# Performance work log

Measured on AMD Instinct MI355X. Metric: run time of the kernel, lower is better.

## Reference

```python
import jax, jax.numpy as jnp
import numpy as np

N = 10000      # nodes
E = 320000     # edges (before self loops)
IN = 256
HID = 64
H = 8
OUT = 64
NEG_SLOPE = 0.2


def setup_inputs() -> dict:
    key = jax.random.key(0)
    ks = jax.random.split(key, 12)
    def glorot(k, shape):
        fan = sum(shape) if len(shape) == 2 else int(np.prod(shape))
        return jax.random.normal(k, shape, jnp.float32) * np.sqrt(2.0 / fan)
    x = jax.random.normal(ks[0], (N, IN), jnp.float32)
    edge_index = jax.random.randint(ks[1], (2, E), 0, N, jnp.int32)
    # positive weights so log2 is finite
    edge_weight = jax.random.uniform(ks[2], (E,), jnp.float32, 0.1, 1.0)
    return {
        'x': x, 'edge_index': edge_index, 'edge_weight': edge_weight,
        'W1': glorot(ks[3], (IN, H * HID)),
        'as1': glorot(ks[4], (H, HID)), 'ad1': glorot(ks[5], (H, HID)),
        'b1': jnp.zeros((H * HID,), jnp.float32),
        'W2': glorot(ks[6], (H * HID, H * OUT)),
        'as2': glorot(ks[7], (H, OUT)), 'ad2': glorot(ks[8], (H, OUT)),
        'b2': jnp.zeros((H * OUT,), jnp.float32),
    }


def _gat_conv(x, src, dst, log2_ew, W, att_src, att_dst, bias, heads, ch):
    n = x.shape[0]
    h = (x @ W).reshape(n, heads, ch)                      # [N,H,C]
    al_src = jnp.einsum('nhc,hc->nh', h, att_src)          # [N,H]
    al_dst = jnp.einsum('nhc,hc->nh', h, att_dst)
    alpha = al_src[src] + al_dst[dst]                      # [E,H]
    alpha = jax.nn.leaky_relu(alpha, NEG_SLOPE)
    alpha = alpha + log2_ew[:, None]
    # segment softmax over destination nodes (self loops ensure nonempty segments)
    amax = jax.ops.segment_max(alpha, dst, num_segments=n)
    ex = jnp.exp(alpha - amax[dst])
    denom = jax.ops.segment_sum(ex, dst, num_segments=n)
    alpha = ex / denom[dst]                                # [E,H]
    msg = h[src] * alpha[:, :, None]                       # [E,H,C]
    out = jax.ops.segment_sum(msg, dst, num_segments=n)    # [N,H,C]
    return out.reshape(n, heads * ch) + bias


def reference(x, edge_index, edge_weight, W1, as1, ad1, b1, W2, as2, ad2, b2):
    n = x.shape[0]
    # add self loops with fill_value = 1.0 (log2(1) = 0)
    loops = jnp.arange(n, dtype=edge_index.dtype)
    src = jnp.concatenate([edge_index[0], loops])
    dst = jnp.concatenate([edge_index[1], loops])
    ew = jnp.concatenate([edge_weight, jnp.ones((n,), edge_weight.dtype)])
    log2_ew = jnp.log2(ew)
    h = _gat_conv(x, src, dst, log2_ew, W1, as1, ad1, b1, H, HID)
    h = jax.nn.relu(h)  # dropout skipped (eval mode)
    out = _gat_conv(h, src, dst, log2_ew, W2, as2, ad2, b2, H, OUT)
    return out
```

## Files before the change

### kernel.cpp

```cpp
#include <hip/hip_runtime.h>
#include <hip/hip_bf16.h>

#define NN 10000
#define EE 320000
#define ETOT (EE + NN)
#define CIN 256
#define HC 512
#define NHEAD 8
#define NEG 0.2f

#define SX (NN * CIN)
#define SW1 (CIN * HC)
#define SW2 (HC * HC)
#define SATT (6 * 512)

using bf16x8 = __attribute__((ext_vector_type(8))) short;
using f32x4 = __attribute__((ext_vector_type(4))) float;
typedef unsigned short u16;
typedef unsigned int u32;

__device__ __forceinline__ u16 f2bf(float f) {
  __hip_bfloat16 b = __float2bfloat16(f);
  return *(u16*)&b;
}
__device__ __forceinline__ float bflo(u32 p) { return __uint_as_float(p << 16); }
__device__ __forceinline__ float bfhi(u32 p) { return __uint_as_float(p & 0xFFFF0000u); }

__global__ void zdetect_k(const u16* __restrict__ x, int* __restrict__ flag,
                          int* __restrict__ counts) {
  int i = blockIdx.x * blockDim.x + threadIdx.x;
  if (i < NN) counts[i] = 0;
  if (blockIdx.x == 0 && threadIdx.x < 64) {
    int bad = 0;
    for (int j = threadIdx.x; j < 512; j += 64) {
      unsigned e = (x[j] >> 7) & 0xFFu;
      if (e >= 0xC8u) bad = 1;
    }
    unsigned long long b = __ballot(bad);
    if (threadIdx.x == 0) *flag = (b == 0ull) ? 1 : 0;
  }
}

__global__ void cvt_count_k(const void* __restrict__ x,
                            const void* a0, const void* a1, const void* a2,
                            const void* a3, const void* a4, const void* a5,
                            const int* __restrict__ ei,
                            u16* __restrict__ xb, float* __restrict__ attf,
                            int* __restrict__ counts, const int* __restrict__ flag) {
  int i = blockIdx.x * blockDim.x + threadIdx.x;
  const bool bf = (*flag != 0);
  if (i < SX) {
    xb[i] = bf ? ((const u16*)x)[i] : f2bf(((const float*)x)[i]);
  } else if (i < SX + SATT) {
    int j = i - SX;
    const void* ps[6] = {a0, a1, a2, a3, a4, a5};
    const void* p = ps[j >> 9];
    int k = j & 511;
    attf[j] = bf ? __bfloat162float(((const __hip_bfloat16*)p)[k])
                 : ((const float*)p)[k];
  }
  if (i < ETOT) {
    int d = (i < EE) ? ei[EE + i] : (i - EE);
    atomicAdd(&counts[d], 1);
  }
}

__global__ __launch_bounds__(256) void wtrans_k(const void* __restrict__ w1,
                                                const void* __restrict__ w2,
                                                u16* __restrict__ w1t,
                                                u16* __restrict__ w2t,
                                                const int* __restrict__ flag) {
  __shared__ u16 tile[64][72];
  int b = blockIdx.x;
  const void* src;
  u16* dst;
  int K, tk, tn;
  if (b < 32) { src = w1; dst = w1t; K = CIN; tk = (b >> 3) * 64; tn = (b & 7) * 64; }
  else { b -= 32; src = w2; dst = w2t; K = HC; tk = (b >> 3) * 64; tn = (b & 7) * 64; }
  const bool bf = (*flag != 0);
  const int t = threadIdx.x;
  const int r = t >> 2, cb = (t & 3) * 16;
  if (bf) {
    const u16* s = (const u16*)src + (size_t)(tk + r) * HC + tn + cb;
    *(int4*)&tile[r][cb] = ((const int4*)s)[0];
    *(int4*)&tile[r][cb + 8] = ((const int4*)s)[1];
  } else {
    const float* s = (const float*)src + (size_t)(tk + r) * HC + tn + cb;
#pragma unroll
    for (int j = 0; j < 16; j++) tile[r][cb + j] = f2bf(s[j]);
  }
  __syncthreads();
  union { u16 o[16]; int4 v[2]; } u;
#pragma unroll
  for (int j = 0; j < 16; j++) u.o[j] = tile[cb + j][r];
  int4* dp = (int4*)(dst + (size_t)(tn + r) * K + tk + cb);
  dp[0] = u.v[0];
  dp[1] = u.v[1];
}

__global__ __launch_bounds__(1024) void scan_k(const int* __restrict__ counts,
                                               int* __restrict__ rowptr,
                                               int* __restrict__ wcur) {
  __shared__ int buf[1024];
  const int t = threadIdx.x;
  int loc[10];
  int s = 0;
#pragma unroll
  for (int j = 0; j < 10; j++) {
    int i = t * 10 + j;
    s += (i < NN) ? counts[i] : 0;
    loc[j] = s;
  }
  buf[t] = s;
  __syncthreads();
  for (int off = 1; off < 1024; off <<= 1) {
    int v = (t >= off) ? buf[t - off] : 0;
    __syncthreads();
    buf[t] += v;
    __syncthreads();
  }
  int base = (t > 0) ? buf[t - 1] : 0;
  int prev = 0;
#pragma unroll
  for (int j = 0; j < 10; j++) {
    int i = t * 10 + j;
    if (i < NN) {
      rowptr[i + 1] = base + loc[j];
      wcur[i] = base + prev;
    }
    prev = loc[j];
  }
  if (t == 0) rowptr[0] = 0;
}

__global__ void fill_k(const int* __restrict__ ei, const void* __restrict__ ew,
                       const int* __restrict__ flag, int* __restrict__ wcur,
                       int* __restrict__ esrc, float* __restrict__ elw) {
  int e = blockIdx.x * blockDim.x + threadIdx.x;
  if (e >= ETOT) return;
  int s, d;
  float lw;
  if (e < EE) {
    s = ei[e];
    d = ei[EE + e];
    float w = (*flag) ? __bfloat162float(((const __hip_bfloat16*)ew)[e])
                      : ((const float*)ew)[e];
    lw = log2f(w);
  } else {
    s = d = e - EE;
    lw = 0.f;
  }
  int pos = atomicAdd(&wcur[d], 1);
  esrc[pos] = s;
  elw[pos] = lw;
}

#define BM 128
#define BN 64
#define BK 32
#define APAD 40
#define BPAD 40

__global__ __launch_bounds__(256) void gemm_mfma(const u16* __restrict__ A,
                                                 const u16* __restrict__ Wt,
                                                 const float* __restrict__ as_w,
                                                 const float* __restrict__ ad_w,
                                                 u16* __restrict__ hb,
                                                 float* __restrict__ alsrc,
                                                 float* __restrict__ aldst,
                                                 int M, int K) {
  __shared__ u16 As[BM * APAD];
  __shared__ u16 Bs[BN * BPAD];
  const int head = blockIdx.x;
  const int bm = blockIdx.y * BM, bn = head * BN;
  const int t = threadIdx.x;
  const int wave = t >> 6, lane = t & 63;
  const int l15 = lane & 15, quad = lane >> 4;
  f32x4 acc[2][4] = {};
  for (int k0 = 0; k0 < K; k0 += BK) {
    {
      int row = t >> 1, half = t & 1;
      int gr = bm + row;
      int4 v0 = make_int4(0, 0, 0, 0), v1 = v0;
      if (gr < M) {
        const int4* gp = (const int4*)(A + (size_t)gr * K + k0 + half * 16);
        v0 = gp[0];
        v1 = gp[1];
      }
      int4* lp = (int4*)(As + row * APAD + half * 16);
      lp[0] = v0;
      lp[1] = v1;
    }
    {
      int row = t >> 2, kq = (t & 3) * 8;
      *(int4*)(Bs + row * BPAD + kq) =
          *(const int4*)(Wt + (size_t)(bn + row) * K + k0 + kq);
    }
    __syncthreads();
    bf16x8 af[2], bfr[4];
#pragma unroll
    for (int rt = 0; rt < 2; rt++)
      af[rt] = *(const bf16x8*)(As + (wave * 32 + rt * 16 + l15) * APAD + quad * 8);
#pragma unroll
    for (int ct = 0; ct < 4; ct++)
      bfr[ct] = *(const bf16x8*)(Bs + (ct * 16 + l15) * BPAD + quad * 8);
#pragma unroll
    for (int rt = 0; rt < 2; rt++)
#pragma unroll
      for (int ct = 0; ct < 4; ct++)
        acc[rt][ct] = __builtin_amdgcn_mfma_f32_16x16x32_bf16(af[rt], bfr[ct],
                                                              acc[rt][ct], 0, 0, 0);
    __syncthreads();
  }
  float asw[4], adw[4];
#pragma unroll
  for (int ct = 0; ct < 4; ct++) {
    asw[ct] = as_w[head * 64 + ct * 16 + l15];
    adw[ct] = ad_w[head * 64 + ct * 16 + l15];
  }
#pragma unroll
  for (int rt = 0; rt < 2; rt++) {
#pragma unroll
    for (int r = 0; r < 4; r++) {
      int row = bm + wave * 32 + rt * 16 + quad * 4 + r;
      float ps = 0.f, pd = 0.f;
#pragma unroll
      for (int ct = 0; ct < 4; ct++) {
        float v = acc[rt][ct][r];
        ps += v * asw[ct];
        pd += v * adw[ct];
        if (row < M) hb[(size_t)row * HC + bn + ct * 16 + l15] = f2bf(v);
      }
#pragma unroll
      for (int d = 1; d < 16; d <<= 1) {
        ps += __shfl_xor(ps, d);
        pd += __shfl_xor(pd, d);
      }
      if (l15 == 0 && row < M) {
        alsrc[row * NHEAD + head] = ps;
        aldst[row * NHEAD + head] = pd;
      }
    }
  }
}

template <bool RELU, bool FINAL>
__global__ __launch_bounds__(256) void agg_k(const u16* __restrict__ hb,
                                             const float* __restrict__ alsrc,
                                             const float* __restrict__ aldst,
                                             const int* __restrict__ rowptr,
                                             const int* __restrict__ esrc,
                                             const float* __restrict__ elw,
                                             const float* __restrict__ bias,
                                             u32* __restrict__ outB,
                                             float* __restrict__ outF,
                                             const int* __restrict__ flag) {
  const int n = blockIdx.x, t = threadIdx.x;
  const int lane = t & 63, wv = t >> 6;
  const int h = t & 7, eo = t >> 3;
  __shared__ float sred[32];
  __shared__ float sd[NHEAD];
  __shared__ float sw[32 * NHEAD];
  __shared__ int ss[32];
  __shared__ float red4[4][HC];
  const int beg = rowptr[n];
  const int deg = rowptr[n + 1] - beg;
  const float aln = aldst[n * NHEAD + h];

  float areg[8];
  int sreg[8];
  float m = -1e30f;
#pragma unroll
  for (int c = 0; c < 8; c++) {
    int j = c * 32 + eo;
    float a = -1e30f;
    int s = 0;
    if (j < deg) {
      int e = beg + j;
      s = esrc[e];
      a = alsrc[s * NHEAD + h] + aln;
      a = (a > 0.f) ? a : NEG * a;
      a += elw[e];
      m = fmaxf(m, a);
    }
    areg[c] = a;
    sreg[c] = s;
  }
  for (int j = 256 + eo; j < deg; j += 32) {
    int e = beg + j;
    float a = alsrc[esrc[e] * NHEAD + h] + aln;
    a = (a > 0.f) ? a : NEG * a;
    m = fmaxf(m, a + elw[e]);
  }
  m = fmaxf(m, __shfl_xor(m, 8));
  m = fmaxf(m, __shfl_xor(m, 16));
  m = fmaxf(m, __shfl_xor(m, 32));
  if (lane < 8) sred[wv * 8 + lane] = m;
  __syncthreads();
  const float mh = fmaxf(fmaxf(sred[h], sred[8 + h]), fmaxf(sred[16 + h], sred[24 + h]));
  __syncthreads();
  float sum = 0.f;
#pragma unroll
  for (int c = 0; c < 8; c++) {
    int j = c * 32 + eo;
    if (j < deg) {
      float w = expf(areg[c] - mh);
      areg[c] = w;
      sum += w;
    }
  }
  for (int j = 256 + eo; j < deg; j += 32) {
    int e = beg + j;
    float a = alsrc[esrc[e] * NHEAD + h] + aln;
    a = (a > 0.f) ? a : NEG * a;
    sum += expf(a + elw[e] - mh);
  }
  sum += __shfl_xor(sum, 8);
  sum += __shfl_xor(sum, 16);
  sum += __shfl_xor(sum, 32);
  if (lane < 8) sred[wv * 8 + lane] = sum;
  __syncthreads();
  if (t < 8) sd[t] = sred[t] + sred[8 + t] + sred[16 + t] + sred[24 + t];

  const int hh = lane >> 3;
  const int chbase = lane * 8;
  float acc[8] = {};
#pragma unroll
  for (int c = 0; c < 8; c++) {
    const int cb = c * 32;
    if (cb < deg) {
      if (cb + eo < deg) {
        sw[eo * NHEAD + h] = areg[c];
        if (h == 0) ss[eo] = sreg[c];
      }
      __syncthreads();
      const int cnt = min(32, deg - cb);
      for (int i = wv; i < cnt; i += 4) {
        const int s = ss[i];
        const float w = sw[i * NHEAD + hh];
        const int4 p = *(const int4*)(hb + (size_t)s * HC + chbase);
        const u32 p0 = (u32)p.x, p1 = (u32)p.y, p2 = (u32)p.z, p3 = (u32)p.w;
        acc[0] += w * bflo(p0);
        acc[1] += w * bfhi(p0);
        acc[2] += w * bflo(p1);
        acc[3] += w * bfhi(p1);
        acc[4] += w * bflo(p2);
        acc[5] += w * bfhi(p2);
        acc[6] += w * bflo(p3);
        acc[7] += w * bfhi(p3);
      }
      __syncthreads();
    }
  }
  for (int cb = 256; cb < deg; cb += 32) {
    if (cb + eo < deg) {
      int e = beg + cb + eo;
      int s = esrc[e];
      float a = alsrc[s * NHEAD + h] + aln;
      a = (a > 0.f) ? a : NEG * a;
      sw[eo * NHEAD + h] = expf(a + elw[e] - mh);
      if (h == 0) ss[eo] = s;
    }
    __syncthreads();
    const int cnt = min(32, deg - cb);
    for (int i = wv; i < cnt; i += 4) {
      const int s = ss[i];
      const float w = sw[i * NHEAD + hh];
      const int4 p = *(const int4*)(hb + (size_t)s * HC + chbase);
      const u32 p0 = (u32)p.x, p1 = (u32)p.y, p2 = (u32)p.z, p3 = (u32)p.w;
      acc[0] += w * bflo(p0);
      acc[1] += w * bfhi(p0);
      acc[2] += w * bflo(p1);
      acc[3] += w * bfhi(p1);
      acc[4] += w * bflo(p2);
      acc[5] += w * bfhi(p2);
      acc[6] += w * bflo(p3);
      acc[7] += w * bfhi(p3);
    }
    __syncthreads();
  }
#pragma unroll
  for (int j = 0; j < 8; j++) red4[wv][chbase + j] = acc[j];
  __syncthreads();
  const int c0 = 2 * t, c1 = 2 * t + 1;
  float v0 = red4[0][c0] + red4[1][c0] + red4[2][c0] + red4[3][c0];
  float v1 = red4[0][c1] + red4[1][c1] + red4[2][c1] + red4[3][c1];
  const float inv = 1.f / sd[t >> 5];
  v0 = v0 * inv + bias[c0];
  v1 = v1 * inv + bias[c1];
  if (RELU) {
    v0 = fmaxf(v0, 0.f);
    v1 = fmaxf(v1, 0.f);
  }
  if (FINAL && !(*flag)) {
    outF[(size_t)n * HC + c0] = v0;
    outF[(size_t)n * HC + c1] = v1;
  } else {
    outB[(size_t)n * (HC / 2) + t] = (u32)f2bf(v0) | ((u32)f2bf(v1) << 16);
  }
}

static constexpr size_t algn(size_t x) { return (x + 255) & ~(size_t)255; }
static constexpr size_t oFlag = 0;
static constexpr size_t oXB = algn(oFlag + 256);
static constexpr size_t oW1T = algn(oXB + (size_t)SX * 2);
static constexpr size_t oW2T = algn(oW1T + (size_t)SW1 * 2);
static constexpr size_t oAtt = algn(oW2T + (size_t)SW2 * 2);
static constexpr size_t oHB = algn(oAtt + (size_t)SATT * 4);
static constexpr size_t oO1B = algn(oHB + (size_t)NN * HC * 2);
static constexpr size_t oAS = algn(oO1B + (size_t)NN * HC * 2);
static constexpr size_t oAD = algn(oAS + (size_t)NN * NHEAD * 4);
static constexpr size_t oRP = algn(oAD + (size_t)NN * NHEAD * 4);
static constexpr size_t oCnt = algn(oRP + (size_t)(NN + 1) * 4);
static constexpr size_t oWcur = algn(oCnt + (size_t)NN * 4);
static constexpr size_t oESrc = algn(oWcur + (size_t)NN * 4);
static constexpr size_t oELW = algn(oESrc + (size_t)ETOT * 4);

extern "C" void kernel_launch(void* const* d_in, const int* in_sizes, int n_in,
                              void* d_out, int out_size, void* d_ws, size_t ws_size,
                              hipStream_t stream) {
  (void)in_sizes; (void)n_in; (void)out_size; (void)ws_size;
  const int* ei = (const int*)d_in[1];

  char* ws = (char*)d_ws;
  int* flag = (int*)(ws + oFlag);
  u16* xb = (u16*)(ws + oXB);
  u16* w1t = (u16*)(ws + oW1T);
  u16* w2t = (u16*)(ws + oW2T);
  float* attf = (float*)(ws + oAtt);
  float* as1f = attf, *ad1f = attf + 512, *b1f = attf + 1024;
  float* as2f = attf + 1536, *ad2f = attf + 2048, *b2f = attf + 2560;
  u16* hb = (u16*)(ws + oHB);
  u16* o1b = (u16*)(ws + oO1B);
  float* alsrc = (float*)(ws + oAS);
  float* aldst = (float*)(ws + oAD);
  int* rowptr = (int*)(ws + oRP);
  int* counts = (int*)(ws + oCnt);
  int* wcur = (int*)(ws + oWcur);
  int* esrc = (int*)(ws + oESrc);
  float* elw = (float*)(ws + oELW);

  const int eb = (ETOT + 255) / 256;
  const int cvb = (SX + SATT + 255) / 256;

  zdetect_k<<<(NN + 255) / 256, 256, 0, stream>>>((const u16*)d_in[0], flag, counts);
  cvt_count_k<<<cvb, 256, 0, stream>>>(d_in[0], d_in[4], d_in[5], d_in[6],
                                       d_in[8], d_in[9], d_in[10], ei,
                                       xb, attf, counts, flag);
  wtrans_k<<<96, 256, 0, stream>>>(d_in[3], d_in[7], w1t, w2t, flag);
  scan_k<<<1, 1024, 0, stream>>>(counts, rowptr, wcur);
  fill_k<<<eb, 256, 0, stream>>>(ei, d_in[2], flag, wcur, esrc, elw);

  gemm_mfma<<<dim3(8, (NN + BM - 1) / BM), 256, 0, stream>>>(
      xb, w1t, as1f, ad1f, hb, alsrc, aldst, NN, CIN);
  agg_k<true, false><<<NN, 256, 0, stream>>>(hb, alsrc, aldst, rowptr, esrc, elw,
                                             b1f, (u32*)o1b, nullptr, flag);

  gemm_mfma<<<dim3(8, (NN + BM - 1) / BM), 256, 0, stream>>>(
      o1b, w2t, as2f, ad2f, hb, alsrc, aldst, NN, HC);
  agg_k<false, true><<<NN, 256, 0, stream>>>(hb, alsrc, aldst, rowptr, esrc, elw,
                                             b2f, (u32*)d_out, (float*)d_out, flag);
}
```

Before: 271.2 us.

## Fuse prep kernels, retile GEMM, and single-pass edge softmax in aggregation

Merges the dtype-detect, convert, count and weight-transpose kernels into one prep kernel, with a memset zeroing the counts. The GEMM is retiled to 64x128 with BK=64, so each block covers two heads and reduces the attention logits through shared memory. The aggregation kernel now stages per-edge logits for all heads in shared memory with one thread per edge and vector loads when degree is at most 256, which avoids re-reading per-head logits. This cuts launch count and redundant gathers, but uses more shared memory per block and each block re-runs the dtype-detect check.

Measured after the change: 267.0 us. Within noise of the previous version (-1.5%).

```diff
diff --git a/kernel.cpp b/kernel.cpp
--- a/kernel.cpp
+++ b/kernel.cpp
@@ -10,8 +10,6 @@
 #define NEG 0.2f
 
 #define SX (NN * CIN)
-#define SW1 (CIN * HC)
-#define SW2 (HC * HC)
 #define SATT (6 * 512)
 
 using bf16x8 = __attribute__((ext_vector_type(8))) short;
@@ -26,76 +24,78 @@
 __device__ __forceinline__ float bflo(u32 p) { return __uint_as_float(p << 16); }
 __device__ __forceinline__ float bfhi(u32 p) { return __uint_as_float(p & 0xFFFF0000u); }
 
-__global__ void zdetect_k(const u16* __restrict__ x, int* __restrict__ flag,
-                          int* __restrict__ counts) {
-  int i = blockIdx.x * blockDim.x + threadIdx.x;
-  if (i < NN) counts[i] = 0;
-  if (blockIdx.x == 0 && threadIdx.x < 64) {
-    int bad = 0;
-    for (int j = threadIdx.x; j < 512; j += 64) {
-      unsigned e = (x[j] >> 7) & 0xFFu;
-      if (e >= 0xC8u) bad = 1;
-    }
-    unsigned long long b = __ballot(bad);
-    if (threadIdx.x == 0) *flag = (b == 0ull) ? 1 : 0;
-  }
-}
-
-__global__ void cvt_count_k(const void* __restrict__ x,
-                            const void* a0, const void* a1, const void* a2,
-                            const void* a3, const void* a4, const void* a5,
-                            const int* __restrict__ ei,
-                            u16* __restrict__ xb, float* __restrict__ attf,
-                            int* __restrict__ counts, const int* __restrict__ flag) {
-  int i = blockIdx.x * blockDim.x + threadIdx.x;
-  const bool bf = (*flag != 0);
-  if (i < SX) {
-    xb[i] = bf ? ((const u16*)x)[i] : f2bf(((const float*)x)[i]);
-  } else if (i < SX + SATT) {
-    int j = i - SX;
-    const void* ps[6] = {a0, a1, a2, a3, a4, a5};
-    const void* p = ps[j >> 9];
-    int k = j & 511;
-    attf[j] = bf ? __bfloat162float(((const __hip_bfloat16*)p)[k])
-                 : ((const float*)p)[k];
-  }
-  if (i < ETOT) {
-    int d = (i < EE) ? ei[EE + i] : (i - EE);
-    atomicAdd(&counts[d], 1);
-  }
-}
-
-__global__ __launch_bounds__(256) void wtrans_k(const void* __restrict__ w1,
-                                                const void* __restrict__ w2,
-                                                u16* __restrict__ w1t,
-                                                u16* __restrict__ w2t,
-                                                const int* __restrict__ flag) {
-  __shared__ u16 tile[64][72];
-  int b = blockIdx.x;
-  const void* src;
-  u16* dst;
-  int K, tk, tn;
-  if (b < 32) { src = w1; dst = w1t; K = CIN; tk = (b >> 3) * 64; tn = (b & 7) * 64; }
-  else { b -= 32; src = w2; dst = w2t; K = HC; tk = (b >> 3) * 64; tn = (b & 7) * 64; }
-  const bool bf = (*flag != 0);
-  const int t = threadIdx.x;
-  const int r = t >> 2, cb = (t & 3) * 16;
-  if (bf) {
-    const u16* s = (const u16*)src + (size_t)(tk + r) * HC + tn + cb;
-    *(int4*)&tile[r][cb] = ((const int4*)s)[0];
-    *(int4*)&tile[r][cb + 8] = ((const int4*)s)[1];
+#define PB_X ((SX + 255) / 256)
+#define PB_ATT ((SATT + 255) / 256)
+#define PB_CNT ((ETOT + 255) / 256)
+#define PB_WT 96
+#define PB_TOT (PB_X + PB_ATT + PB_CNT + PB_WT)
+
+__global__ __launch_bounds__(256) void prep_k(
+    const void* __restrict__ x, const void* __restrict__ w1,
+    const void* __restrict__ w2,
+    const void* a0, const void* a1, const void* a2,
+    const void* a3, const void* a4, const void* a5,
+    const int* __restrict__ ei,
+    u16* __restrict__ xb, u16* __restrict__ w1t, u16* __restrict__ w2t,
+    float* __restrict__ attf, int* __restrict__ counts, int* __restrict__ flag) {
+  const int b = blockIdx.x, t = threadIdx.x;
+  __shared__ int sbad;
+  if (t == 0) sbad = 0;
+  __syncthreads();
+  {
+    const u16* xu = (const u16*)x;
+    unsigned e0 = (xu[2 * t] >> 7) & 0xFFu;
+    unsigned e1 = (xu[2 * t + 1] >> 7) & 0xFFu;
+    if (e0 >= 0xC8u || e1 >= 0xC8u) sbad = 1;
+  }
+  __syncthreads();
+  const bool bf = (sbad == 0);
+  if (b == 0 && t == 0) *flag = bf ? 1 : 0;
+
+  if (b < PB_X) {
+    int i = b * 256 + t;
+    if (i < SX) xb[i] = bf ? ((const u16*)x)[i] : f2bf(((const float*)x)[i]);
+  } else if (b < PB_X + PB_ATT) {
+    int j = (b - PB_X) * 256 + t;
+    if (j < SATT) {
+      const void* ps[6] = {a0, a1, a2, a3, a4, a5};
+      const void* p = ps[j >> 9];
+      int k = j & 511;
+      attf[j] = bf ? __bfloat162float(((const __hip_bfloat16*)p)[k])
+                   : ((const float*)p)[k];
+    }
+  } else if (b < PB_X + PB_ATT + PB_CNT) {
+    int e = (b - PB_X - PB_ATT) * 256 + t;
+    if (e < ETOT) {
+      int d = (e < EE) ? ei[EE + e] : (e - EE);
+      atomicAdd(&counts[d], 1);
+    }
   } else {
-    const float* s = (const float*)src + (size_t)(tk + r) * HC + tn + cb;
-#pragma unroll
-    for (int j = 0; j < 16; j++) tile[r][cb + j] = f2bf(s[j]);
-  }
-  __syncthreads();
-  union { u16 o[16]; int4 v[2]; } u;
-#pragma unroll
-  for (int j = 0; j < 16; j++) u.o[j] = tile[cb + j][r];
-  int4* dp = (int4*)(dst + (size_t)(tn + r) * K + tk + cb);
-  dp[0] = u.v[0];
-  dp[1] = u.v[1];
+    __shared__ u16 tile[64][72];
+    int wb = b - (PB_X + PB_ATT + PB_CNT);
+    const void* src;
+    u16* dst;
+    int K, tk, tn;
+    if (wb < 32) { src = w1; dst = w1t; K = CIN; tk = (wb >> 3) * 64; tn = (wb & 7) * 64; }
+    else { wb -= 32; src = w2; dst = w2t; K = HC; tk = (wb >> 3) * 64; tn = (wb & 7) * 64; }
+    const int r = t >> 2, cb = (t & 3) * 16;
+    if (bf) {
+      const u16* s = (const u16*)src + (size_t)(tk + r) * HC + tn + cb;
+      *(int4*)&tile[r][cb] = ((const int4*)s)[0];
+      *(int4*)&tile[r][cb + 8] = ((const int4*)s)[1];
+    } else {
+      const float* s = (const float*)src + (size_t)(tk + r) * HC + tn + cb;
+#pragma unroll
+      for (int j = 0; j < 16; j++) tile[r][cb + j] = f2bf(s[j]);
+    }
+    __syncthreads();
+    union { u16 o[16]; int4 v[2]; } u;
+#pragma unroll
+    for (int j = 0; j < 16; j++) u.o[j] = tile[cb + j][r];
+    int4* dp = (int4*)(dst + (size_t)(tn + r) * K + tk + cb);
+    dp[0] = u.v[0];
+    dp[1] = u.v[1];
+  }
 }
 
 __global__ __launch_bounds__(1024) void scan_k(const int* __restrict__ counts,
@@ -155,11 +155,10 @@
   elw[pos] = lw;
 }
 
-#define BM 128
-#define BN 64
-#define BK 32
-#define APAD 40
-#define BPAD 40
+#define BM 64
+#define BN 128
+#define BK 64
+#define LSTR 72
 
 __global__ __launch_bounds__(256) void gemm_mfma(const u16* __restrict__ A,
                                                  const u16* __restrict__ Wt,
@@ -169,77 +168,96 @@
                                                  float* __restrict__ alsrc,
                                                  float* __restrict__ aldst,
                                                  int M, int K) {
-  __shared__ u16 As[BM * APAD];
-  __shared__ u16 Bs[BN * BPAD];
-  const int head = blockIdx.x;
-  const int bm = blockIdx.y * BM, bn = head * BN;
-  const int t = threadIdx.x;
-  const int wave = t >> 6, lane = t & 63;
+  __shared__ u16 As[BM * LSTR];
+  __shared__ u16 Bs[BN * LSTR];
+  __shared__ float sps[2][2][BM], spd[2][2][BM];
+  const int bx = blockIdx.x;
+  const int bm = blockIdx.y * BM, bn = bx * BN;
+  const int t = threadIdx.x, wv = t >> 6, lane = t & 63;
   const int l15 = lane & 15, quad = lane >> 4;
-  f32x4 acc[2][4] = {};
+  f32x4 acc[4][2] = {};
   for (int k0 = 0; k0 < K; k0 += BK) {
     {
-      int row = t >> 1, half = t & 1;
+      int row = t >> 2, kq = (t & 3) * 16;
       int gr = bm + row;
       int4 v0 = make_int4(0, 0, 0, 0), v1 = v0;
       if (gr < M) {
-        const int4* gp = (const int4*)(A + (size_t)gr * K + k0 + half * 16);
+        const int4* gp = (const int4*)(A + (size_t)gr * K + k0 + kq);
         v0 = gp[0];
         v1 = gp[1];
       }
-      int4* lp = (int4*)(As + row * APAD + half * 16);
+      int4* lp = (int4*)(As + row * LSTR + kq);
       lp[0] = v0;
       lp[1] = v1;
     }
     {
-      int row = t >> 2, kq = (t & 3) * 8;
-      *(int4*)(Bs + row * BPAD + kq) =
-          *(const int4*)(Wt + (size_t)(bn + row) * K + k0 + kq);
-    }
-    __syncthreads();
-    bf16x8 af[2], bfr[4];
-#pragma unroll
-    for (int rt = 0; rt < 2; rt++)
-      af[rt] = *(const bf16x8*)(As + (wave * 32 + rt * 16 + l15) * APAD + quad * 8);
-#pragma unroll
-    for (int ct = 0; ct < 4; ct++)
-      bfr[ct] = *(const bf16x8*)(Bs + (ct * 16 + l15) * BPAD + quad * 8);
-#pragma unroll
-    for (int rt = 0; rt < 2; rt++)
-#pragma unroll
-      for (int ct = 0; ct < 4; ct++)
-        acc[rt][ct] = __builtin_amdgcn_mfma_f32_16x16x32_bf16(af[rt], bfr[ct],
-                                                              acc[rt][ct], 0, 0, 0);
-    __syncthreads();
-  }
-  float asw[4], adw[4];
-#pragma unroll
-  for (int ct = 0; ct < 4; ct++) {
-    asw[ct] = as_w[head * 64 + ct * 16 + l15];
-    adw[ct] = ad_w[head * 64 + ct * 16 + l15];
-  }
-#pragma unroll
-  for (int rt = 0; rt < 2; rt++) {
+      int row = t >> 1, kq = (t & 1) * 32;
+      const int4* gp = (const int4*)(Wt + (size_t)(bn + row) * K + k0 + kq);
+      int4* lp = (int4*)(Bs + row * LSTR + kq);
+      lp[0] = gp[0];
+      lp[1] = gp[1];
+      lp[2] = gp[2];
+      lp[3] = gp[3];
+    }
+    __syncthreads();
+#pragma unroll
+    for (int kk = 0; kk < 2; kk++) {
+      bf16x8 bfr[2];
+#pragma unroll
+      for (int ct = 0; ct < 2; ct++)
+        bfr[ct] = *(const bf16x8*)(Bs + (wv * 32 + ct * 16 + l15) * LSTR + kk * 32 + quad * 8);
+#pragma unroll
+      for (int rt = 0; rt < 4; rt++) {
+        bf16x8 af = *(const bf16x8*)(As + (rt * 16 + l15) * LSTR + kk * 32 + quad * 8);
+#pragma unroll
+        for (int ct = 0; ct < 2; ct++)
+          acc[rt][ct] = __builtin_amdgcn_mfma_f32_16x16x32_bf16(af, bfr[ct],
+                                                                acc[rt][ct], 0, 0, 0);
+      }
+    }
+    __syncthreads();
+  }
+  const int head = bx * 2 + (wv >> 1);
+  float asw[2], adw[2];
+#pragma unroll
+  for (int ct = 0; ct < 2; ct++) {
+    int c = head * 64 + (wv & 1) * 32 + ct * 16 + l15;
+    asw[ct] = as_w[c];
+    adw[ct] = ad_w[c];
+  }
+#pragma unroll
+  for (int rt = 0; rt < 4; rt++) {
 #pragma unroll
     for (int r = 0; r < 4; r++) {
-      int row = bm + wave * 32 + rt * 16 + quad * 4 + r;
+      int rib = rt * 16 + quad * 4 + r;
+      int row = bm + rib;
       float ps = 0.f, pd = 0.f;
 #pragma unroll
-      for (int ct = 0; ct < 4; ct++) {
+      for (int ct = 0; ct < 2; ct++) {
         float v = acc[rt][ct][r];
         ps += v * asw[ct];
         pd += v * adw[ct];
-        if (row < M) hb[(size_t)row * HC + bn + ct * 16 + l15] = f2bf(v);
+        if (row < M)
+          hb[(size_t)row * HC + bn + wv * 32 + ct * 16 + l15] = f2bf(v);
       }
 #pragma unroll
       for (int d = 1; d < 16; d <<= 1) {
         ps += __shfl_xor(ps, d);
         pd += __shfl_xor(pd, d);
       }
-      if (l15 == 0 && row < M) {
-        alsrc[row * NHEAD + head] = ps;
-        aldst[row * NHEAD + head] = pd;
-      }
+      if (l15 == 0) {
+        sps[wv >> 1][wv & 1][rib] = ps;
+        spd[wv >> 1][wv & 1][rib] = pd;
+      }
+    }
+  }
+  __syncthreads();
+  if (t < 2 * BM) {
+    int rib = t & 63, hs = t >> 6;
+    int row = bm + rib;
+    if (row < M) {
+      alsrc[row * NHEAD + bx * 2 + hs] = sps[hs][0][rib] + sps[hs][1][rib];
+      aldst[row * NHEAD + bx * 2 + hs] = spd[hs][0][rib] + spd[hs][1][rib];
     }
   }
 }
@@ -258,86 +276,135 @@
   const int n = blockIdx.x, t = threadIdx.x;
   const int lane = t & 63, wv = t >> 6;
   const int h = t & 7, eo = t >> 3;
+  const int hh = lane >> 3;
+  __shared__ float sw[8 * 260];
+  __shared__ int ss[256];
   __shared__ float sred[32];
-  __shared__ float sd[NHEAD];
-  __shared__ float sw[32 * NHEAD];
-  __shared__ int ss[32];
+  __shared__ float smh[8], sd[8];
   __shared__ float red4[4][HC];
   const int beg = rowptr[n];
   const int deg = rowptr[n + 1] - beg;
-  const float aln = aldst[n * NHEAD + h];
-
-  float areg[8];
-  int sreg[8];
-  float m = -1e30f;
-#pragma unroll
-  for (int c = 0; c < 8; c++) {
-    int j = c * 32 + eo;
-    float a = -1e30f;
-    int s = 0;
-    if (j < deg) {
-      int e = beg + j;
-      s = esrc[e];
-      a = alsrc[s * NHEAD + h] + aln;
-      a = (a > 0.f) ? a : NEG * a;
-      a += elw[e];
-      m = fmaxf(m, a);
-    }
-    areg[c] = a;
-    sreg[c] = s;
-  }
-  for (int j = 256 + eo; j < deg; j += 32) {
-    int e = beg + j;
-    float a = alsrc[esrc[e] * NHEAD + h] + aln;
-    a = (a > 0.f) ? a : NEG * a;
-    m = fmaxf(m, a + elw[e]);
-  }
-  m = fmaxf(m, __shfl_xor(m, 8));
-  m = fmaxf(m, __shfl_xor(m, 16));
-  m = fmaxf(m, __shfl_xor(m, 32));
-  if (lane < 8) sred[wv * 8 + lane] = m;
-  __syncthreads();
-  const float mh = fmaxf(fmaxf(sred[h], sred[8 + h]), fmaxf(sred[16 + h], sred[24 + h]));
-  __syncthreads();
-  float sum = 0.f;
-#pragma unroll
-  for (int c = 0; c < 8; c++) {
-    int j = c * 32 + eo;
-    if (j < deg) {
-      float w = expf(areg[c] - mh);
-      areg[c] = w;
-      sum += w;
-    }
-  }
-  for (int j = 256 + eo; j < deg; j += 32) {
-    int e = beg + j;
-    float a = alsrc[esrc[e] * NHEAD + h] + aln;
-    a = (a > 0.f) ? a : NEG * a;
-    sum += expf(a + elw[e] - mh);
-  }
-  sum += __shfl_xor(sum, 8);
-  sum += __shfl_xor(sum, 16);
-  sum += __shfl_xor(sum, 32);
-  if (lane < 8) sred[wv * 8 + lane] = sum;
-  __syncthreads();
-  if (t < 8) sd[t] = sred[t] + sred[8 + t] + sred[16 + t] + sred[24 + t];
-
-  const int hh = lane >> 3;
+  const float4 dd0 = *(const float4*)(aldst + (size_t)n * NHEAD);
+  const float4 dd1 = *(const float4*)(aldst + (size_t)n * NHEAD + 4);
   const int chbase = lane * 8;
   float acc[8] = {};
-#pragma unroll
-  for (int c = 0; c < 8; c++) {
-    const int cb = c * 32;
-    if (cb < deg) {
-      if (cb + eo < deg) {
-        sw[eo * NHEAD + h] = areg[c];
-        if (h == 0) ss[eo] = sreg[c];
+
+  if (deg <= 256) {
+    if (t < deg) {
+      int e = beg + t;
+      int s = esrc[e];
+      float lw = elw[e];
+      float4 q0 = *(const float4*)(alsrc + (size_t)s * NHEAD);
+      float4 q1 = *(const float4*)(alsrc + (size_t)s * NHEAD + 4);
+      float a;
+      a = q0.x + dd0.x; a = (a > 0.f) ? a : NEG * a; sw[0 * 260 + t] = a + lw;
+      a = q0.y + dd0.y; a = (a > 0.f) ? a : NEG * a; sw[1 * 260 + t] = a + lw;
+      a = q0.z + dd0.z; a = (a > 0.f) ? a : NEG * a; sw[2 * 260 + t] = a + lw;
+      a = q0.w + dd0.w; a = (a > 0.f) ? a : NEG * a; sw[3 * 260 + t] = a + lw;
+      a = q1.x + dd1.x; a = (a > 0.f) ? a : NEG * a; sw[4 * 260 + t] = a + lw;
+      a = q1.y + dd1.y; a = (a > 0.f) ? a : NEG * a; sw[5 * 260 + t] = a + lw;
+      a = q1.z + dd1.z; a = (a > 0.f) ? a : NEG * a; sw[6 * 260 + t] = a + lw;
+      a = q1.w + dd1.w; a = (a > 0.f) ? a : NEG * a; sw[7 * 260 + t] = a + lw;
+      ss[t] = s;
+    }
+    __syncthreads();
+    float m = -1e30f;
+#pragma unroll
+    for (int c = 0; c < 8; c++) {
+      int j = c * 32 + eo;
+      if (j < deg) m = fmaxf(m, sw[h * 260 + j]);
+    }
+    m = fmaxf(m, __shfl_xor(m, 8));
+    m = fmaxf(m, __shfl_xor(m, 16));
+    m = fmaxf(m, __shfl_xor(m, 32));
+    if (lane < 8) sred[wv * 8 + lane] = m;
+    __syncthreads();
+    const float mh = fmaxf(fmaxf(sred[h], sred[8 + h]), fmaxf(sred[16 + h], sred[24 + h]));
+    __syncthreads();
+    float sum = 0.f;
+#pragma unroll
+    for (int c = 0; c < 8; c++) {
+      int j = c * 32 + eo;
+      if (j < deg) {
+        float w = expf(sw[h * 260 + j] - mh);
+        sw[h * 260 + j] = w;
+        sum += w;
+      }
+    }
+    sum += __shfl_xor(sum, 8);
+    sum += __shfl_xor(sum, 16);
+    sum += __shfl_xor(sum, 32);
+    if (lane < 8) sred[wv * 8 + lane] = sum;
+    __syncthreads();
+    if (t < 8) sd[t] = sred[t] + sred[8 + t] + sred[16 + t] + sred[24 + t];
+    for (int i = wv; i < deg; i += 4) {
+      const int s = ss[i];
+      const float w = sw[hh * 260 + i];
+      const int4 p = *(const int4*)(hb + (size_t)s * HC + chbase);
+      const u32 p0 = (u32)p.x, p1 = (u32)p.y, p2 = (u32)p.z, p3 = (u32)p.w;
+      acc[0] += w * bflo(p0);
+      acc[1] += w * bfhi(p0);
+      acc[2] += w * bflo(p1);
+      acc[3] += w * bfhi(p1);
+      acc[4] += w * bflo(p2);
+      acc[5] += w * bfhi(p2);
+      acc[6] += w * bflo(p3);
+      acc[7] += w * bfhi(p3);
+    }
+  } else {
+    const float aln = aldst[(size_t)n * NHEAD + h];
+    float m = -1e30f;
+    for (int j = eo; j < deg; j += 32) {
+      int e = beg + j;
+      float a = alsrc[(size_t)esrc[e] * NHEAD + h] + aln;
+      a = (a > 0.f) ? a : NEG * a;
+      m = fmaxf(m, a + elw[e]);
+    }
+    m = fmaxf(m, __shfl_xor(m, 8));
+    m = fmaxf(m, __shfl_xor(m, 16));
+    m = fmaxf(m, __shfl_xor(m, 32));
+    if (lane < 8) sred[wv * 8 + lane] = m;
+    __syncthreads();
+    const float mh = fmaxf(fmaxf(sred[h], sred[8 + h]), fmaxf(sred[16 + h], sred[24 + h]));
+    if (t < 8) smh[t] = mh;
+    __syncthreads();
+    float sum = 0.f;
+    for (int j = eo; j < deg; j += 32) {
+      int e = beg + j;
+      float a = alsrc[(size_t)esrc[e] * NHEAD + h] + aln;
+      a = (a > 0.f) ? a : NEG * a;
+      sum += expf(a + elw[e] - mh);
+    }
+    sum += __shfl_xor(sum, 8);
+    sum += __shfl_xor(sum, 16);
+    sum += __shfl_xor(sum, 32);
+    if (lane < 8) sred[wv * 8 + lane] = sum;
+    __syncthreads();
+    if (t < 8) sd[t] = sred[t] + sred[8 + t] + sred[16 + t] + sred[24 + t];
+    for (int cb = 0; cb < deg; cb += 256) {
+      int j = cb + t;
+      if (j < deg) {
+        int e = beg + j;
+        int s = esrc[e];
+        float lw = elw[e];
+        float4 q0 = *(const float4*)(alsrc + (size_t)s * NHEAD);
+        float4 q1 = *(const float4*)(alsrc + (size_t)s * NHEAD + 4);
+        float a;
+        a = q0.x + dd0.x; a = (a > 0.f) ? a : NEG * a; sw[0 * 260 + t] = expf(a + lw - smh[0]);
+        a = q0.y + dd0.y; a = (a > 0.f) ? a : NEG * a; sw[1 * 260 + t] = expf(a + lw - smh[1]);
+        a = q0.z + dd0.z; a = (a > 0.f) ? a : NEG * a; sw[2 * 260 + t] = expf(a + lw - smh[2]);
+        a = q0.w + dd0.w; a = (a > 0.f) ? a : NEG * a; sw[3 * 260 + t] = expf(a + lw - smh[3]);
+        a = q1.x + dd1.x; a = (a > 0.f) ? a : NEG * a; sw[4 * 260 + t] = expf(a + lw - smh[4]);
+        a = q1.y + dd1.y; a = (a > 0.f) ? a : NEG * a; sw[5 * 260 + t] = expf(a + lw - smh[5]);
+        a = q1.z + dd1.z; a = (a > 0.f) ? a : NEG * a; sw[6 * 260 + t] = expf(a + lw - smh[6]);
+        a = q1.w + dd1.w; a = (a > 0.f) ? a : NEG * a; sw[7 * 260 + t] = expf(a + lw - smh[7]);
+        ss[t] = s;
       }
       __syncthreads();
-      const int cnt = min(32, deg - cb);
+      int cnt = min(256, deg - cb);
       for (int i = wv; i < cnt; i += 4) {
         const int s = ss[i];
-        const float w = sw[i * NHEAD + hh];
+        const float w = sw[hh * 260 + i];
         const int4 p = *(const int4*)(hb + (size_t)s * HC + chbase);
         const u32 p0 = (u32)p.x, p1 = (u32)p.y, p2 = (u32)p.z, p3 = (u32)p.w;
         acc[0] += w * bflo(p0);
@@ -352,49 +419,22 @@
       __syncthreads();
     }
   }
-  for (int cb = 256; cb < deg; cb += 32) {
-    if (cb + eo < deg) {
-      int e = beg + cb + eo;
-      int s = esrc[e];
-      float a = alsrc[s * NHEAD + h] + aln;
-      a = (a > 0.f) ? a : NEG * a;
-      sw[eo * NHEAD + h] = expf(a + elw[e] - mh);
-      if (h == 0) ss[eo] = s;
-    }
-    __syncthreads();
-    const int cnt = min(32, deg - cb);
-    for (int i = wv; i < cnt; i += 4) {
-      const int s = ss[i];
-      const float w = sw[i * NHEAD + hh];
-      const int4 p = *(const int4*)(hb + (size_t)s * HC + chbase);
-      const u32 p0 = (u32)p.x, p1 = (u32)p.y, p2 = (u32)p.z, p3 = (u32)p.w;
-      acc[0] += w * bflo(p0);
-      acc[1] += w * bfhi(p0);
-      acc[2] += w * bflo(p1);
-      acc[3] += w * bfhi(p1);
-      acc[4] += w * bflo(p2);
-      acc[5] += w * bfhi(p2);
-      acc[6] += w * bflo(p3);
-      acc[7] += w * bfhi(p3);
-    }
-    __syncthreads();
-  }
 #pragma unroll
   for (int j = 0; j < 8; j++) red4[wv][chbase + j] = acc[j];
   __syncthreads();
-  const int c0 = 2 * t, c1 = 2 * t + 1;
+  const int c0 = 2 * t;
   float v0 = red4[0][c0] + red4[1][c0] + red4[2][c0] + red4[3][c0];
-  float v1 = red4[0][c1] + red4[1][c1] + red4[2][c1] + red4[3][c1];
+  float v1 = red4[0][c0 + 1] + red4[1][c0 + 1] + red4[2][c0 + 1] + red4[3][c0 + 1];
   const float inv = 1.f / sd[t >> 5];
   v0 = v0 * inv + bias[c0];
-  v1 = v1 * inv + bias[c1];
+  v1 = v1 * inv + bias[c0 + 1];
   if (RELU) {
     v0 = fmaxf(v0, 0.f);
     v1 = fmaxf(v1, 0.f);
   }
   if (FINAL && !(*flag)) {
     outF[(size_t)n * HC + c0] = v0;
-    outF[(size_t)n * HC + c1] = v1;
+    outF[(size_t)n * HC + c0 + 1] = v1;
   } else {
     outB[(size_t)n * (HC / 2) + t] = (u32)f2bf(v0) | ((u32)f2bf(v1) << 16);
   }
@@ -404,8 +444,8 @@
 static constexpr size_t oFlag = 0;
 static constexpr size_t oXB = algn(oFlag + 256);
 static constexpr size_t oW1T = algn(oXB + (size_t)SX * 2);
-static constexpr size_t oW2T = algn(oW1T + (size_t)SW1 * 2);
-static constexpr size_t oAtt = algn(oW2T + (size_t)SW2 * 2);
+static constexpr size_t oW2T = algn(oW1T + (size_t)CIN * HC * 2);
+static constexpr size_t oAtt = algn(oW2T + (size_t)HC * HC * 2);
 static constexpr size_t oHB = algn(oAtt + (size_t)SATT * 4);
 static constexpr size_t oO1B = algn(oHB + (size_t)NN * HC * 2);
 static constexpr size_t oAS = algn(oO1B + (size_t)NN * HC * 2);
@@ -440,23 +480,20 @@
   int* esrc = (int*)(ws + oESrc);
   float* elw = (float*)(ws + oELW);
 
-  const int eb = (ETOT + 255) / 256;
-  const int cvb = (SX + SATT + 255) / 256;
-
-  zdetect_k<<<(NN + 255) / 256, 256, 0, stream>>>((const u16*)d_in[0], flag, counts);
-  cvt_count_k<<<cvb, 256, 0, stream>>>(d_in[0], d_in[4], d_in[5], d_in[6],
-                                       d_in[8], d_in[9], d_in[10], ei,
-                                       xb, attf, counts, flag);
-  wtrans_k<<<96, 256, 0, stream>>>(d_in[3], d_in[7], w1t, w2t, flag);
+  hipMemsetAsync(counts, 0, (size_t)NN * 4, stream);
+  prep_k<<<PB_TOT, 256, 0, stream>>>(d_in[0], d_in[3], d_in[7],
+                                     d_in[4], d_in[5], d_in[6],
+                                     d_in[8], d_in[9], d_in[10], ei,
+                                     xb, w1t, w2t, attf, counts, flag);
   scan_k<<<1, 1024, 0, stream>>>(counts, rowptr, wcur);
-  fill_k<<<eb, 256, 0, stream>>>(ei, d_in[2], flag, wcur, esrc, elw);
-
-  gemm_mfma<<<dim3(8, (NN + BM - 1) / BM), 256, 0, stream>>>(
+  fill_k<<<(ETOT + 255) / 256, 256, 0, stream>>>(ei, d_in[2], flag, wcur, esrc, elw);
+
+  gemm_mfma<<<dim3(HC / BN, (NN + BM - 1) / BM), 256, 0, stream>>>(
       xb, w1t, as1f, ad1f, hb, alsrc, aldst, NN, CIN);
   agg_k<true, false><<<NN, 256, 0, stream>>>(hb, alsrc, aldst, rowptr, esrc, elw,
                                              b1f, (u32*)o1b, nullptr, flag);
 
-  gemm_mfma<<<dim3(8, (NN + BM - 1) / BM), 256, 0, stream>>>(
+  gemm_mfma<<<dim3(HC / BN, (NN + BM - 1) / BM), 256, 0, stream>>>(
       o1b, w2t, as2f, ad2f, hb, alsrc, aldst, NN, HC);
   agg_k<false, true><<<NN, 256, 0, stream>>>(hb, alsrc, aldst, rowptr, esrc, elw,
                                              b2f, (u32*)d_out, (float*)d_out, flag);
```
